# Kernel tuning notes

Hardware: AMD Instinct MI355X
Metric: run time of the kernel (lower is better)

## Reference

```python
import jax, jax.numpy as jnp
import numpy as np

jax.config.update("jax_enable_x64", True)  # original casts the recurrence to float64

FS = 100.0          # sampling rate (fs init kwarg)
CHUNK = 500         # int(5 * fs)
TAU_MIN = 2.001 / FS


def setup_inputs() -> dict:
    key = jax.random.key(0)
    k1, k2, k3 = jax.random.split(key, 3)
    B, T, U = 8, 50000, 16
    inputs = jax.random.normal(k1, (B, T, U), dtype=jnp.float32)
    u = jax.random.normal(k2, (U,), dtype=jnp.float32) * 0.05
    tau = jax.random.normal(k3, (U,), dtype=jnp.float32) * 0.05
    return {"inputs": inputs, "u": u, "tau": tau}


def _cumtrapz(z):
    # trapezoidal cumulative integral along axis 1, initial value 0 (dx=1)
    mid = (z[:, :-1] + z[:, 1:]) * 0.5
    mid = jnp.pad(mid, ((0, 0), (1, 0), (0, 0)))
    return jnp.cumsum(mid, axis=1)


def _stp_forward(inputs, u, tau):
    B, T, U = inputs.shape
    tstim = jnp.where(jnp.isnan(inputs), 0.0, inputs)
    # weight constraints (u_constraint=abs, tau_constraint=max(abs, 2.001/fs)),
    # then call() takes abs again (idempotent)
    ui = jnp.abs(u) / FS * 100.0                      # (U,)
    taui = jnp.maximum(jnp.abs(tau), TAU_MIN) * FS    # (U,)
    a = (1.0 / taui).astype(jnp.float64)[None, None, :]   # (1,1,U)
    x = (ui[None, None, :] * tstim).astype(jnp.float64)   # (B,T,U)

    n_chunks = T // CHUNK  # T chosen as a multiple of CHUNK (no reset_signal)
    xc = x.reshape(B, n_chunks, CHUNK, U).transpose(1, 0, 2, 3)  # (nc,B,C,U)

    carry0 = (jnp.zeros((B, 1, U), jnp.float64),  # x0
              jnp.zeros((B, 1, U), jnp.float64))  # imu0

    def step(carry, xi):
        x0, imu0 = carry
        ix = _cumtrapz(a + xi) + a + (x0 + xi[:, :1]) * 0.5
        mu = jnp.exp(ix)
        imu = _cumtrapz(mu * xi) + (x0 + mu[:, :1] * xi[:, :1]) * 0.5 + imu0
        valid = (mu > 0.0) & (imu > 0.0)
        mu_s = jnp.where(valid, mu, 1.0)
        imu_s = jnp.where(valid, imu, 1.0)
        td = jnp.where(valid, 1.0 - jnp.exp(jnp.log(imu_s) - jnp.log(mu_s)), 1.0)
        new_carry = (xi[:, -1:], imu_s[:, -1:] / mu_s[:, -1:])
        return new_carry, td

    _, td = jax.lax.scan(step, carry0, xc)  # (nc,B,C,U)
    td = td.transpose(1, 0, 2, 3).reshape(B, T, U).astype(jnp.float32)

    # shift td by one sample (prepend 1.0), multiply by stimulus
    td_shift = jnp.pad(td[:, :-1, :], ((0, 0), (1, 0), (0, 0)), constant_values=1.0)
    ret = tstim * td_shift
    return jnp.where(jnp.isnan(inputs), 0.0, ret)


def reference(inputs, u, tau):
    return _stp_forward(inputs, u, tau)
```

## Files before the change

kernel.cpp:

```cpp
#include <hip/hip_runtime.h>
#include <math.h>


#define TDIM 50000
#define UDIM 16
#define NCH 100
#define SEG 20
#define SLEN 25
#define NSEQ 128

struct alignas(16) PQt { double P; double Q; };

__device__ __forceinline__ float clean(float v) { return (v != v) ? 0.0f : v; }

__device__ __forceinline__ double exp_small(double y) {
    double p = 2.08767569878681e-9;
    p = fma(p, y, 2.505210838544172e-8);
    p = fma(p, y, 2.755731922398589e-7);
    p = fma(p, y, 2.7557319223985893e-6);
    p = fma(p, y, 2.48015873015873e-5);
    p = fma(p, y, 1.984126984126984e-4);
    p = fma(p, y, 1.3888888888888889e-3);
    p = fma(p, y, 8.333333333333333e-3);
    p = fma(p, y, 4.1666666666666664e-2);
    p = fma(p, y, 1.6666666666666666e-1);
    p = fma(p, y, 0.5);
    p = fma(p, y, 1.0);
    p = fma(p, y, 1.0);
    return p;
}

__global__ __launch_bounds__(320, 4) void stp_kA(
    const float* __restrict__ inp, const float* __restrict__ uu,
    const float* __restrict__ tauv, PQt* __restrict__ PQ,
    double* __restrict__ rraw)
{
    const int c = blockIdx.x >> 3;
    const int b = blockIdx.x & 7;
    const int s = threadIdx.x >> 4;
    const int u = threadIdx.x & 15;
    const int n0 = c * 500 + s * SLEN;

    const float ui   = (fabsf(uu[u]) / 100.0f) * 100.0f;
    const float taui = fmaxf(fabsf(tauv[u]), 0.02001f) * 100.0f;
    const double a   = (double)(1.0f / taui);
    const double ea  = exp(-a);

    const float* p = inp + ((size_t)b * TDIM + n0) * UDIM + u;
    double xp = (n0 != 0) ? (double)(ui * clean(p[-UDIM])) : 0.0;
    double ep = exp_small(-0.5 * xp);
    double A = 1.0, B = 0.0;

#pragma unroll 5
    for (int t = 0; t < SLEN; ++t) {
        const double x  = (double)(ui * clean(p[(size_t)t * UDIM]));
        const double ex = exp_small(-0.5 * x);
        const double e  = ea * ep * ex;
        A *= e;
        B = fma(e, fma(xp, 0.5, B), 0.5 * x);
        ep = ex; xp = x;
    }

    __shared__ double sA[SEG][16];
    __shared__ double sB[SEG][16];
    sA[s][u] = A;
    sB[s][u] = B;
    __syncthreads();

    double P = 1.0, Q = 0.0;
    for (int j = 0; j < s; ++j) {
        const double Aj = sA[j][u];
        const double Bj = sB[j][u];
        P *= Aj;
        Q = fma(Aj, Q, Bj);
    }

    const int sbu = b * 16 + u;
    PQ[((size_t)c * SEG + s) * NSEQ + sbu] = {P, Q};
    if (s == SEG - 1) {
        rraw[(size_t)c * NSEQ + sbu] = fma(A, Q, B);
    }
}

__global__ __launch_bounds__(128, 4) void stp_kB(
    const float* __restrict__ inp, const float* __restrict__ uu,
    const float* __restrict__ tauv, const PQt* __restrict__ PQ,
    const double* __restrict__ rraw, float* __restrict__ out)
{
    const int tid = blockIdx.x * 128 + threadIdx.x;
    const int sbu = tid & (NSEQ - 1);
    const int seg = tid >> 7;
    const int c   = seg / SEG;
    const int s   = seg - c * SEG;
    const int u   = sbu & 15;
    const int b   = sbu >> 4;
    const int n0  = seg * SLEN;

    const float ui   = (fabsf(uu[u]) / 100.0f) * 100.0f;
    const float taui = fmaxf(fabsf(tauv[u]), 0.02001f) * 100.0f;
    const float af   = 1.0f / taui;

    const PQt pq = PQ[(size_t)seg * NSEQ + sbu];
    double carry = 0.0, tdp_d = 1.0;
    if (c > 0) {
        const double re = rraw[(size_t)(c - 1) * NSEQ + sbu];
        carry = (re > 0.0) ? re : 1.0;
        tdp_d = (re > 0.0) ? 1.0 - re : 1.0;
    }
    const double r_in = fma(pq.P, carry, pq.Q);
    if (s > 0) tdp_d = (r_in > 0.0) ? 1.0 - r_in : 1.0;

    const float* p = inp + ((size_t)b * TDIM + n0) * UDIM + u;
    float*       o = out + ((size_t)b * TDIM + n0) * UDIM + u;
    float xp = (n0 != 0) ? ui * clean(p[-UDIM]) : 0.0f;

    float r   = (float)r_in;
    float tdp = (float)tdp_d;
#pragma unroll 5
    for (int t = 0; t < SLEN; ++t) {
        const float ts = clean(p[(size_t)t * UDIM]);
        const float x  = ui * ts;
        const float d  = af + (xp + x) * 0.5f;
        const float e  = __expf(-d);
        r = e * (r + xp * 0.5f) + x * 0.5f;
        o[(size_t)t * UDIM] = ts * tdp;
        tdp = (r > 0.0f) ? 1.0f - r : 1.0f;
        xp = x;
    }
}

extern "C" void kernel_launch(void* const* d_in, const int* in_sizes, int n_in,
                              void* d_out, int out_size, void* d_ws, size_t ws_size,
                              hipStream_t stream) {
    const float* inp  = (const float*)d_in[0];
    const float* uu   = (const float*)d_in[1];
    const float* tauv = (const float*)d_in[2];
    float* out = (float*)d_out;

    PQt*    PQ   = (PQt*)d_ws;
    double* rraw = (double*)((char*)d_ws + 4096000);

    stp_kA<<<dim3(NCH * 8), dim3(320), 0, stream>>>(inp, uu, tauv, PQ, rraw);
    stp_kB<<<dim3(2000), dim3(128), 0, stream>>>(inp, uu, tauv, PQ, rraw, out);
}
```

Measured before the change: 25.91 us.

## Fuse both passes into one cooperative kernel with a grid-wide sync

Combines the segment-summary pass and the output pass into a single cooperative kernel. Each thread keeps its prefix (P,Q) in registers, and the two passes are separated by a grid sync instead of a second launch and a round trip through the PQ workspace. This removes one kernel launch and the PQ global traffic. In exchange it adds grid-synchronisation cost and needs all 800 blocks to be co-resident; if that check or the cooperative launch fails, it falls back to the two-kernel path.

```diff
diff --git a/kernel.cpp b/kernel.cpp
--- a/kernel.cpp
+++ b/kernel.cpp
@@ -1,5 +1,8 @@
 #include <hip/hip_runtime.h>
+#include <hip/hip_cooperative_groups.h>
 #include <math.h>
+
+namespace cg = cooperative_groups;
 
 
 #define TDIM 50000
@@ -30,6 +33,86 @@
     return p;
 }
 
+__global__ __launch_bounds__(320, 5) void stp_fused(
+    const float* __restrict__ inp, const float* __restrict__ uu,
+    const float* __restrict__ tauv, double* __restrict__ rraw,
+    float* __restrict__ out)
+{
+    const int c = blockIdx.x >> 3;
+    const int b = blockIdx.x & 7;
+    const int s = threadIdx.x >> 4;
+    const int u = threadIdx.x & 15;
+    const int n0 = c * 500 + s * SLEN;
+
+    const float ui   = (fabsf(uu[u]) / 100.0f) * 100.0f;
+    const float taui = fmaxf(fabsf(tauv[u]), 0.02001f) * 100.0f;
+    const float af   = 1.0f / taui;
+    const double a   = (double)af;
+    const double ea  = exp(-a);
+
+    const float* p = inp + ((size_t)b * TDIM + n0) * UDIM + u;
+
+    double xp = (n0 != 0) ? (double)(ui * clean(p[-UDIM])) : 0.0;
+    double ep = exp_small(-0.5 * xp);
+    double A = 1.0, B = 0.0;
+#pragma unroll 5
+    for (int t = 0; t < SLEN; ++t) {
+        const double x  = (double)(ui * clean(p[(size_t)t * UDIM]));
+        const double ex = exp_small(-0.5 * x);
+        const double e  = ea * ep * ex;
+        A *= e;
+        B = fma(e, fma(xp, 0.5, B), 0.5 * x);
+        ep = ex; xp = x;
+    }
+
+    __shared__ double sA[SEG][16];
+    __shared__ double sB[SEG][16];
+    sA[s][u] = A;
+    sB[s][u] = B;
+    __syncthreads();
+
+    double P = 1.0, Q = 0.0;
+    for (int j = 0; j < s; ++j) {
+        const double Aj = sA[j][u];
+        const double Bj = sB[j][u];
+        P *= Aj;
+        Q = fma(Aj, Q, Bj);
+    }
+    const int sbu = b * 16 + u;
+    if (s == SEG - 1) {
+        rraw[(size_t)c * NSEQ + sbu] = fma(A, Q, B);
+    }
+
+    __threadfence();
+    cg::this_grid().sync();
+
+    double carry = 0.0, tdp_d = 1.0;
+    if (c > 0) {
+        const double re = rraw[(size_t)(c - 1) * NSEQ + sbu];
+        carry = (re > 0.0) ? re : 1.0;
+        tdp_d = (re > 0.0) ? 1.0 - re : 1.0;
+    }
+    const double r_in = fma(P, carry, Q);
+    if (s > 0) tdp_d = (r_in > 0.0) ? 1.0 - r_in : 1.0;
+
+    float* o = out + ((size_t)b * TDIM + n0) * UDIM + u;
+    float xpf = (n0 != 0) ? ui * clean(p[-UDIM]) : 0.0f;
+    float r   = (float)r_in;
+    float tdp = (float)tdp_d;
+#pragma unroll 5
+    for (int t = 0; t < SLEN; ++t) {
+        const float ts = clean(p[(size_t)t * UDIM]);
+        const float x  = ui * ts;
+        const float d  = af + (xpf + x) * 0.5f;
+        const float e  = __expf(-d);
+        r = e * (r + xpf * 0.5f) + x * 0.5f;
+        o[(size_t)t * UDIM] = ts * tdp;
+        tdp = (r > 0.0f) ? 1.0f - r : 1.0f;
+        xpf = x;
+    }
+}
+
+
 __global__ __launch_bounds__(320, 4) void stp_kA(
     const float* __restrict__ inp, const float* __restrict__ uu,
     const float* __restrict__ tauv, PQt* __restrict__ PQ,
@@ -50,7 +133,6 @@
     double xp = (n0 != 0) ? (double)(ui * clean(p[-UDIM])) : 0.0;
     double ep = exp_small(-0.5 * xp);
     double A = 1.0, B = 0.0;
-
 #pragma unroll 5
     for (int t = 0; t < SLEN; ++t) {
         const double x  = (double)(ui * clean(p[(size_t)t * UDIM]));
@@ -77,9 +159,7 @@
 
     const int sbu = b * 16 + u;
     PQ[((size_t)c * SEG + s) * NSEQ + sbu] = {P, Q};
-    if (s == SEG - 1) {
-        rraw[(size_t)c * NSEQ + sbu] = fma(A, Q, B);
-    }
+    if (s == SEG - 1) rraw[(size_t)c * NSEQ + sbu] = fma(A, Q, B);
 }
 
 __global__ __launch_bounds__(128, 4) void stp_kB(
@@ -140,6 +220,17 @@
     PQt*    PQ   = (PQt*)d_ws;
     double* rraw = (double*)((char*)d_ws + 4096000);
 
+    int maxB = 0;
+    hipError_t qerr = hipOccupancyMaxActiveBlocksPerMultiprocessor(
+        &maxB, stp_fused, 320, 0);
+    if (qerr == hipSuccess && maxB * 256 >= NCH * 8) {
+        void* args[] = { (void*)&inp, (void*)&uu, (void*)&tauv,
+                         (void*)&rraw, (void*)&out };
+        hipError_t lerr = hipLaunchCooperativeKernel(
+            (const void*)stp_fused, dim3(NCH * 8), dim3(320), args, 0, stream);
+        if (lerr == hipSuccess) return;
+    }
+
     stp_kA<<<dim3(NCH * 8), dim3(320), 0, stream>>>(inp, uu, tauv, PQ, rraw);
     stp_kB<<<dim3(2000), dim3(128), 0, stream>>>(inp, uu, tauv, PQ, rraw, out);
 }
```

Result: no change. 25.93 us (+0.1%).

## Fuse two-pass chunk scan into one kernel by recomputing previous chunk's scan

Applied to the files above, without the earlier changes.

Merges the two kernels into a single launch. Each block recomputes the previous chunk's segment transfer coefficients in double precision to get the incoming carry, so the workspace round trip and second launch are no longer needed. The carry still holds because chunk boundaries reset the recurrence apart from the previous chunk's final ratio. The exp polynomial is also shortened by one term and the exp(-a) call swapped for the polynomial. In exchange the double-precision work in the first phase roughly doubles and there is a small change in accuracy.

```diff
diff --git a/kernel.cpp b/kernel.cpp
--- a/kernel.cpp
+++ b/kernel.cpp
@@ -9,15 +9,12 @@
 #define SLEN 25
 #define NSEQ 128
 
-struct alignas(16) PQt { double P; double Q; };
-
 __device__ __forceinline__ float clean(float v) { return (v != v) ? 0.0f : v; }
 
 __device__ __forceinline__ double exp_small(double y) {
-    double p = 2.08767569878681e-9;
-    p = fma(p, y, 2.505210838544172e-8);
-    p = fma(p, y, 2.755731922398589e-7);
-    p = fma(p, y, 2.7557319223985893e-6);
+    double p = 2.505210838544172e-8;
+    p = fma(p, y, 2.7557319223985893e-7);
+    p = fma(p, y, 2.755731922398589e-6);
     p = fma(p, y, 2.48015873015873e-5);
     p = fma(p, y, 1.984126984126984e-4);
     p = fma(p, y, 1.3888888888888889e-3);
@@ -30,102 +27,88 @@
     return p;
 }
 
-__global__ __launch_bounds__(320, 4) void stp_kA(
+__global__ __launch_bounds__(320, 4) void stp_one(
     const float* __restrict__ inp, const float* __restrict__ uu,
-    const float* __restrict__ tauv, PQt* __restrict__ PQ,
-    double* __restrict__ rraw)
+    const float* __restrict__ tauv, float* __restrict__ out)
 {
     const int c = blockIdx.x >> 3;
     const int b = blockIdx.x & 7;
     const int s = threadIdx.x >> 4;
     const int u = threadIdx.x & 15;
-    const int n0 = c * 500 + s * SLEN;
+    const int cm1 = (c > 0) ? c - 1 : 0;
+    const int n0R = c   * 500 + s * SLEN;
+    const int n0L = cm1 * 500 + s * SLEN;
 
     const float ui   = (fabsf(uu[u]) / 100.0f) * 100.0f;
     const float taui = fmaxf(fabsf(tauv[u]), 0.02001f) * 100.0f;
-    const double a   = (double)(1.0f / taui);
-    const double ea  = exp(-a);
+    const float af   = 1.0f / taui;
+    const double a   = (double)af;
+    const double ea  = exp_small(-a);
 
-    const float* p = inp + ((size_t)b * TDIM + n0) * UDIM + u;
-    double xp = (n0 != 0) ? (double)(ui * clean(p[-UDIM])) : 0.0;
-    double ep = exp_small(-0.5 * xp);
-    double A = 1.0, B = 0.0;
+    const float* pL = inp + ((size_t)b * TDIM + n0L) * UDIM + u;
+    const float* pR = inp + ((size_t)b * TDIM + n0R) * UDIM + u;
 
+    double xpL = (n0L != 0) ? (double)(ui * clean(pL[-UDIM])) : 0.0;
+    double xpR = (n0R != 0) ? (double)(ui * clean(pR[-UDIM])) : 0.0;
+    double epL = exp_small(-0.5 * xpL);
+    double epR = exp_small(-0.5 * xpR);
+    double AL = 1.0, BL = 0.0, AR = 1.0, BR = 0.0;
 #pragma unroll 5
     for (int t = 0; t < SLEN; ++t) {
-        const double x  = (double)(ui * clean(p[(size_t)t * UDIM]));
-        const double ex = exp_small(-0.5 * x);
-        const double e  = ea * ep * ex;
-        A *= e;
-        B = fma(e, fma(xp, 0.5, B), 0.5 * x);
-        ep = ex; xp = x;
+        const double xL  = (double)(ui * clean(pL[(size_t)t * UDIM]));
+        const double xR  = (double)(ui * clean(pR[(size_t)t * UDIM]));
+        const double exL = exp_small(-0.5 * xL);
+        const double exR = exp_small(-0.5 * xR);
+        const double eL  = ea * epL * exL;
+        const double eR  = ea * epR * exR;
+        AL *= eL;  BL = fma(eL, fma(xpL, 0.5, BL), 0.5 * xL);
+        AR *= eR;  BR = fma(eR, fma(xpR, 0.5, BR), 0.5 * xR);
+        epL = exL; epR = exR; xpL = xL; xpR = xR;
     }
 
-    __shared__ double sA[SEG][16];
-    __shared__ double sB[SEG][16];
-    sA[s][u] = A;
-    sB[s][u] = B;
+    __shared__ double sAL[SEG][16], sBL[SEG][16];
+    __shared__ double sAR[SEG][16], sBR[SEG][16];
+    sAL[s][u] = AL; sBL[s][u] = BL;
+    sAR[s][u] = AR; sBR[s][u] = BR;
     __syncthreads();
+
+    double rp = 0.0;
+#pragma unroll
+    for (int j = 0; j < SEG; ++j) rp = fma(sAL[j][u], rp, sBL[j][u]);
 
     double P = 1.0, Q = 0.0;
     for (int j = 0; j < s; ++j) {
-        const double Aj = sA[j][u];
-        const double Bj = sB[j][u];
+        const double Aj = sAR[j][u];
+        const double Bj = sBR[j][u];
         P *= Aj;
         Q = fma(Aj, Q, Bj);
     }
 
-    const int sbu = b * 16 + u;
-    PQ[((size_t)c * SEG + s) * NSEQ + sbu] = {P, Q};
-    if (s == SEG - 1) {
-        rraw[(size_t)c * NSEQ + sbu] = fma(A, Q, B);
+    double carry, tdp_d;
+    if (c > 0) {
+        carry = (rp > 0.0) ? rp : 1.0;
+        tdp_d = (rp > 0.0) ? 1.0 - rp : 1.0;
+    } else {
+        carry = 0.0;
+        tdp_d = 1.0;
     }
-}
-
-__global__ __launch_bounds__(128, 4) void stp_kB(
-    const float* __restrict__ inp, const float* __restrict__ uu,
-    const float* __restrict__ tauv, const PQt* __restrict__ PQ,
-    const double* __restrict__ rraw, float* __restrict__ out)
-{
-    const int tid = blockIdx.x * 128 + threadIdx.x;
-    const int sbu = tid & (NSEQ - 1);
-    const int seg = tid >> 7;
-    const int c   = seg / SEG;
-    const int s   = seg - c * SEG;
-    const int u   = sbu & 15;
-    const int b   = sbu >> 4;
-    const int n0  = seg * SLEN;
-
-    const float ui   = (fabsf(uu[u]) / 100.0f) * 100.0f;
-    const float taui = fmaxf(fabsf(tauv[u]), 0.02001f) * 100.0f;
-    const float af   = 1.0f / taui;
-
-    const PQt pq = PQ[(size_t)seg * NSEQ + sbu];
-    double carry = 0.0, tdp_d = 1.0;
-    if (c > 0) {
-        const double re = rraw[(size_t)(c - 1) * NSEQ + sbu];
-        carry = (re > 0.0) ? re : 1.0;
-        tdp_d = (re > 0.0) ? 1.0 - re : 1.0;
-    }
-    const double r_in = fma(pq.P, carry, pq.Q);
+    const double r_in = fma(P, carry, Q);
     if (s > 0) tdp_d = (r_in > 0.0) ? 1.0 - r_in : 1.0;
 
-    const float* p = inp + ((size_t)b * TDIM + n0) * UDIM + u;
-    float*       o = out + ((size_t)b * TDIM + n0) * UDIM + u;
-    float xp = (n0 != 0) ? ui * clean(p[-UDIM]) : 0.0f;
-
+    float* o = out + ((size_t)b * TDIM + n0R) * UDIM + u;
+    float xpf = (n0R != 0) ? ui * clean(pR[-UDIM]) : 0.0f;
     float r   = (float)r_in;
     float tdp = (float)tdp_d;
 #pragma unroll 5
     for (int t = 0; t < SLEN; ++t) {
-        const float ts = clean(p[(size_t)t * UDIM]);
+        const float ts = clean(pR[(size_t)t * UDIM]);
         const float x  = ui * ts;
-        const float d  = af + (xp + x) * 0.5f;
+        const float d  = af + (xpf + x) * 0.5f;
         const float e  = __expf(-d);
-        r = e * (r + xp * 0.5f) + x * 0.5f;
+        r = e * (r + xpf * 0.5f) + x * 0.5f;
         o[(size_t)t * UDIM] = ts * tdp;
         tdp = (r > 0.0f) ? 1.0f - r : 1.0f;
-        xp = x;
+        xpf = x;
     }
 }
 
@@ -137,9 +120,5 @@
     const float* tauv = (const float*)d_in[2];
     float* out = (float*)d_out;
 
-    PQt*    PQ   = (PQt*)d_ws;
-    double* rraw = (double*)((char*)d_ws + 4096000);
-
-    stp_kA<<<dim3(NCH * 8), dim3(320), 0, stream>>>(inp, uu, tauv, PQ, rraw);
-    stp_kB<<<dim3(2000), dim3(128), 0, stream>>>(inp, uu, tauv, PQ, rraw, out);
+    stp_one<<<dim3(NCH * 8), dim3(320), 0, stream>>>(inp, uu, tauv, out);
 }
```

Measured after the change: 29.67 us. 14.5% more time.

## Process four units per thread with float4 loads in both scan kernels

Applied to the files above, without the earlier changes.

Each thread now handles four adjacent units, so inputs are read and outputs written as float4 vectors. Threads per problem drop fourfold, and both launch grids are reshaped to match (200 and 250 blocks). The double-precision exp polynomial loses one term and ea now uses it in place of exp(). This trades fewer, wider memory operations for less thread parallelism and longer dependent chains per thread, which may expose latency on a device with many CUs.

```diff
diff --git a/kernel.cpp b/kernel.cpp
--- a/kernel.cpp
+++ b/kernel.cpp
@@ -11,13 +11,19 @@
 
 struct alignas(16) PQt { double P; double Q; };
 
-__device__ __forceinline__ float clean(float v) { return (v != v) ? 0.0f : v; }
+__device__ __forceinline__ float cleanf(float v) { return (v != v) ? 0.0f : v; }
+__device__ __forceinline__ float4 clean4(float4 v) {
+    v.x = cleanf(v.x); v.y = cleanf(v.y); v.z = cleanf(v.z); v.w = cleanf(v.w);
+    return v;
+}
+__device__ __forceinline__ float getc(const float4& v, int j) {
+    return j == 0 ? v.x : (j == 1 ? v.y : (j == 2 ? v.z : v.w));
+}
 
 __device__ __forceinline__ double exp_small(double y) {
-    double p = 2.08767569878681e-9;
-    p = fma(p, y, 2.505210838544172e-8);
-    p = fma(p, y, 2.755731922398589e-7);
-    p = fma(p, y, 2.7557319223985893e-6);
+    double p = 2.505210838544172e-8;
+    p = fma(p, y, 2.7557319223985893e-7);
+    p = fma(p, y, 2.755731922398589e-6);
     p = fma(p, y, 2.48015873015873e-5);
     p = fma(p, y, 1.984126984126984e-4);
     p = fma(p, y, 1.3888888888888889e-3);
@@ -30,102 +36,157 @@
     return p;
 }
 
-__global__ __launch_bounds__(320, 4) void stp_kA(
+__global__ __launch_bounds__(320) void stp_kA(
     const float* __restrict__ inp, const float* __restrict__ uu,
     const float* __restrict__ tauv, PQt* __restrict__ PQ,
     double* __restrict__ rraw)
 {
-    const int c = blockIdx.x >> 3;
-    const int b = blockIdx.x & 7;
-    const int s = threadIdx.x >> 4;
-    const int u = threadIdx.x & 15;
-    const int n0 = c * 500 + s * SLEN;
-
-    const float ui   = (fabsf(uu[u]) / 100.0f) * 100.0f;
-    const float taui = fmaxf(fabsf(tauv[u]), 0.02001f) * 100.0f;
-    const double a   = (double)(1.0f / taui);
-    const double ea  = exp(-a);
-
-    const float* p = inp + ((size_t)b * TDIM + n0) * UDIM + u;
-    double xp = (n0 != 0) ? (double)(ui * clean(p[-UDIM])) : 0.0;
-    double ep = exp_small(-0.5 * xp);
-    double A = 1.0, B = 0.0;
-
+    const int c    = blockIdx.x >> 1;
+    const int half = blockIdx.x & 1;
+    const int tid  = threadIdx.x;
+    const int bl   = tid / 80;
+    const int rem  = tid - bl * 80;
+    const int s    = rem >> 2;
+    const int q    = rem & 3;
+    const int b    = half * 4 + bl;
+    const int u0   = q * 4;
+    const int n0   = c * 500 + s * SLEN;
+
+    float uif[4]; double ea[4];
+    #pragma unroll
+    for (int j = 0; j < 4; ++j) {
+        const int u = u0 + j;
+        uif[j] = (fabsf(uu[u]) / 100.0f) * 100.0f;
+        const float taui = fmaxf(fabsf(tauv[u]), 0.02001f) * 100.0f;
+        ea[j] = exp_small(-(double)(1.0f / taui));
+    }
+
+    const float4* p4 = (const float4*)(inp + ((size_t)b * TDIM + n0) * UDIM + u0);
+
+    double xp[4], ep[4], A[4], B[4];
+    {
+        float4 xv = make_float4(0.f, 0.f, 0.f, 0.f);
+        if (n0 != 0) xv = clean4(p4[-4]);
+        #pragma unroll
+        for (int j = 0; j < 4; ++j) {
+            xp[j] = (double)(uif[j] * getc(xv, j));
+            ep[j] = exp_small(-0.5 * xp[j]);
+            A[j] = 1.0; B[j] = 0.0;
+        }
+    }
 #pragma unroll 5
     for (int t = 0; t < SLEN; ++t) {
-        const double x  = (double)(ui * clean(p[(size_t)t * UDIM]));
-        const double ex = exp_small(-0.5 * x);
-        const double e  = ea * ep * ex;
-        A *= e;
-        B = fma(e, fma(xp, 0.5, B), 0.5 * x);
-        ep = ex; xp = x;
-    }
-
-    __shared__ double sA[SEG][16];
-    __shared__ double sB[SEG][16];
-    sA[s][u] = A;
-    sB[s][u] = B;
+        const float4 v = clean4(p4[t * 4]);
+        #pragma unroll
+        for (int j = 0; j < 4; ++j) {
+            const double x  = (double)(uif[j] * getc(v, j));
+            const double ex = exp_small(-0.5 * x);
+            const double e  = ea[j] * ep[j] * ex;
+            A[j] *= e;
+            B[j] = fma(e, fma(xp[j], 0.5, B[j]), 0.5 * x);
+            ep[j] = ex; xp[j] = x;
+        }
+    }
+
+    __shared__ double sA[4][SEG][16];
+    __shared__ double sB[4][SEG][16];
+    #pragma unroll
+    for (int j = 0; j < 4; ++j) { sA[bl][s][u0 + j] = A[j]; sB[bl][s][u0 + j] = B[j]; }
     __syncthreads();
 
-    double P = 1.0, Q = 0.0;
-    for (int j = 0; j < s; ++j) {
-        const double Aj = sA[j][u];
-        const double Bj = sB[j][u];
-        P *= Aj;
-        Q = fma(Aj, Q, Bj);
-    }
-
-    const int sbu = b * 16 + u;
-    PQ[((size_t)c * SEG + s) * NSEQ + sbu] = {P, Q};
+    double P[4] = {1.0, 1.0, 1.0, 1.0}, Q[4] = {0.0, 0.0, 0.0, 0.0};
+    for (int k = 0; k < s; ++k) {
+        #pragma unroll
+        for (int j = 0; j < 4; ++j) {
+            const double Ak = sA[bl][k][u0 + j];
+            const double Bk = sB[bl][k][u0 + j];
+            P[j] *= Ak;
+            Q[j] = fma(Ak, Q[j], Bk);
+        }
+    }
+
+    const int sbu = b * 16 + u0;
+    PQt* dst = PQ + (size_t)(c * SEG + s) * NSEQ + sbu;
+    #pragma unroll
+    for (int j = 0; j < 4; ++j) { dst[j].P = P[j]; dst[j].Q = Q[j]; }
     if (s == SEG - 1) {
-        rraw[(size_t)c * NSEQ + sbu] = fma(A, Q, B);
-    }
-}
-
-__global__ __launch_bounds__(128, 4) void stp_kB(
+        #pragma unroll
+        for (int j = 0; j < 4; ++j)
+            rraw[(size_t)c * NSEQ + sbu + j] = fma(A[j], Q[j], B[j]);
+    }
+}
+
+__global__ __launch_bounds__(256) void stp_kB(
     const float* __restrict__ inp, const float* __restrict__ uu,
     const float* __restrict__ tauv, const PQt* __restrict__ PQ,
     const double* __restrict__ rraw, float* __restrict__ out)
 {
-    const int tid = blockIdx.x * 128 + threadIdx.x;
-    const int sbu = tid & (NSEQ - 1);
-    const int seg = tid >> 7;
+    const int g   = blockIdx.x * 256 + threadIdx.x;
+    const int q   = g & 3;
+    const int b   = (g >> 2) & 7;
+    const int seg = g >> 5;
     const int c   = seg / SEG;
     const int s   = seg - c * SEG;
-    const int u   = sbu & 15;
-    const int b   = sbu >> 4;
+    const int u0  = q * 4;
+    const int sbu = b * 16 + u0;
     const int n0  = seg * SLEN;
 
-    const float ui   = (fabsf(uu[u]) / 100.0f) * 100.0f;
-    const float taui = fmaxf(fabsf(tauv[u]), 0.02001f) * 100.0f;
-    const float af   = 1.0f / taui;
-
-    const PQt pq = PQ[(size_t)seg * NSEQ + sbu];
-    double carry = 0.0, tdp_d = 1.0;
-    if (c > 0) {
-        const double re = rraw[(size_t)(c - 1) * NSEQ + sbu];
-        carry = (re > 0.0) ? re : 1.0;
-        tdp_d = (re > 0.0) ? 1.0 - re : 1.0;
-    }
-    const double r_in = fma(pq.P, carry, pq.Q);
-    if (s > 0) tdp_d = (r_in > 0.0) ? 1.0 - r_in : 1.0;
-
-    const float* p = inp + ((size_t)b * TDIM + n0) * UDIM + u;
-    float*       o = out + ((size_t)b * TDIM + n0) * UDIM + u;
-    float xp = (n0 != 0) ? ui * clean(p[-UDIM]) : 0.0f;
-
-    float r   = (float)r_in;
-    float tdp = (float)tdp_d;
+    float uif[4], aff[4];
+    #pragma unroll
+    for (int j = 0; j < 4; ++j) {
+        const int u = u0 + j;
+        uif[j] = (fabsf(uu[u]) / 100.0f) * 100.0f;
+        const float taui = fmaxf(fabsf(tauv[u]), 0.02001f) * 100.0f;
+        aff[j] = 1.0f / taui;
+    }
+
+    const PQt* pq = PQ + (size_t)seg * NSEQ + sbu;
+    float r[4], tdp[4];
+    #pragma unroll
+    for (int j = 0; j < 4; ++j) {
+        double carry, tdp_d;
+        if (c > 0) {
+            const double re = rraw[(size_t)(c - 1) * NSEQ + sbu + j];
+            carry = (re > 0.0) ? re : 1.0;
+            tdp_d = (re > 0.0) ? 1.0 - re : 1.0;
+        } else {
+            carry = 0.0;
+            tdp_d = 1.0;
+        }
+        const double r_in = fma(pq[j].P, carry, pq[j].Q);
+        if (s > 0) tdp_d = (r_in > 0.0) ? 1.0 - r_in : 1.0;
+        r[j] = (float)r_in;
+        tdp[j] = (float)tdp_d;
+    }
+
+    const float4* p4 = (const float4*)(inp + ((size_t)b * TDIM + n0) * UDIM + u0);
+    float4*       o4 = (float4*)(out + ((size_t)b * TDIM + n0) * UDIM + u0);
+
+    float xpf[4];
+    {
+        float4 xv = make_float4(0.f, 0.f, 0.f, 0.f);
+        if (n0 != 0) xv = clean4(p4[-4]);
+        #pragma unroll
+        for (int j = 0; j < 4; ++j) xpf[j] = uif[j] * getc(xv, j);
+    }
 #pragma unroll 5
     for (int t = 0; t < SLEN; ++t) {
-        const float ts = clean(p[(size_t)t * UDIM]);
-        const float x  = ui * ts;
-        const float d  = af + (xp + x) * 0.5f;
-        const float e  = __expf(-d);
-        r = e * (r + xp * 0.5f) + x * 0.5f;
-        o[(size_t)t * UDIM] = ts * tdp;
-        tdp = (r > 0.0f) ? 1.0f - r : 1.0f;
-        xp = x;
+        const float4 v = clean4(p4[t * 4]);
+        float4 st;
+        #pragma unroll
+        for (int j = 0; j < 4; ++j) {
+            const float ts = getc(v, j);
+            const float x  = uif[j] * ts;
+            const float d  = aff[j] + (xpf[j] + x) * 0.5f;
+            const float e  = __expf(-d);
+            r[j] = e * (r[j] + xpf[j] * 0.5f) + x * 0.5f;
+            const float ov = ts * tdp[j];
+            tdp[j] = (r[j] > 0.0f) ? 1.0f - r[j] : 1.0f;
+            xpf[j] = x;
+            if (j == 0) st.x = ov; else if (j == 1) st.y = ov;
+            else if (j == 2) st.z = ov; else st.w = ov;
+        }
+        o4[t * 4] = st;
     }
 }
 
@@ -140,6 +201,6 @@
     PQt*    PQ   = (PQt*)d_ws;
     double* rraw = (double*)((char*)d_ws + 4096000);
 
-    stp_kA<<<dim3(NCH * 8), dim3(320), 0, stream>>>(inp, uu, tauv, PQ, rraw);
-    stp_kB<<<dim3(2000), dim3(128), 0, stream>>>(inp, uu, tauv, PQ, rraw, out);
-}
+    stp_kA<<<dim3(200), dim3(320), 0, stream>>>(inp, uu, tauv, PQ, rraw);
+    stp_kB<<<dim3(250), dim3(256), 0, stream>>>(inp, uu, tauv, PQ, rraw, out);
+}
```

Result: slower. 32.59 us (+25.8%).
